# Optimization experiments

Hardware: AMD Instinct MI355X
Metric: run time of the kernel (lower is better)

Reference implementation:

```python
import jax, jax.numpy as jnp
import numpy as np

# pywt db4 decomposition filters
DEC_LO = jnp.array([-0.010597401784997278, 0.032883011666982945, 0.030841381835986965, -0.18703481171888114, -0.02798376941698385, 0.6308807679295904, 0.7148465705525415, 0.23037781330885523], dtype=jnp.float32)
DEC_HI = jnp.array([-0.23037781330885523, 0.7148465705525415, -0.6308807679295904, -0.02798376941698385, 0.18703481171888114, 0.030841381835986965, -0.032883011666982945, -0.010597401784997278], dtype=jnp.float32)

def _dwt_step(x):
    # single-level DWT along last axis, pywt 'symmetric' mode; x: [N, n]
    L = DEC_LO.shape[0]
    xe = jnp.pad(x, ((0, 0), (L - 1, L - 1)), mode='symmetric')[:, 1:]
    k = jnp.stack([DEC_LO[::-1], DEC_HI[::-1]])[:, None, :]  # [2,1,L]
    y = jax.lax.conv_general_dilated(xe[:, None, :], k, window_strides=(2,), padding='VALID')
    return y[:, 0, :], y[:, 1, :]  # cA, cD, each [N, (n+L-1)//2]

def _wavedec(x, level):
    a, dets = x, []
    for _ in range(level):
        a, d = _dwt_step(a)
        dets.append(d)
    return [a] + dets[::-1]  # [cA_L, cD_L, ..., cD_1]

def _wavelet_kan(x, basis, scales=5):
    # torch code detaches x before pywt.wavedec -> stop_gradient for faithful bwd
    coeffs = _wavedec(jax.lax.stop_gradient(x), scales - 1)
    out = 0.0
    for s in range(scales):
        c = coeffs[s]
        out = out + c @ basis[s][:c.shape[1], :]
    return out

def _dendritic(x, W, b):
    # W: [branches, in, out]; max over branches of GELU(Linear)
    h = jnp.einsum('ni,kio->kno', x, W) + b[:, None, :]
    return jnp.max(jax.nn.gelu(h, approximate=False), axis=0)

def _layernorm(x, g, b, eps=1e-5):
    m = jnp.mean(x, -1, keepdims=True)
    v = jnp.var(x, -1, keepdims=True)
    return (x - m) * jax.lax.rsqrt(v + eps) * g + b

def setup_inputs():
    key = jax.random.key(0)
    ks = jax.random.split(key, 12)
    N, D, H, M, Z, K, E = 16384, 768, 512, 256, 256, 20, 262144
    inp = {}
    inp['x'] = jax.random.normal(ks[0], (N, D), jnp.float32)
    inp['adj_rows'] = jax.random.randint(ks[1], (E,), 0, N, jnp.int32)
    inp['adj_cols'] = jax.random.randint(ks[2], (E,), 0, N, jnp.int32)
    inp['adj_vals'] = jax.random.uniform(ks[3], (E,), jnp.float32)
    inp['basis_enc'] = jax.random.normal(ks[4], (5, D, H), jnp.float32)
    inp['ln_g'] = jnp.ones((H,), jnp.float32)
    inp['ln_b'] = jnp.zeros((H,), jnp.float32)
    inp['Wd_enc'] = jax.random.normal(ks[5], (K, H, M), jnp.float32) * 0.04
    inp['bd_enc'] = jnp.zeros((K, M), jnp.float32)
    inp['W_mu'] = jax.random.normal(ks[6], (M, Z), jnp.float32) * 0.06
    inp['b_mu'] = jnp.zeros((Z,), jnp.float32)
    inp['W_lv'] = jax.random.normal(ks[7], (M, Z), jnp.float32) * 0.06
    inp['b_lv'] = jnp.zeros((Z,), jnp.float32)
    inp['Wd_dec'] = jax.random.normal(ks[8], (K, Z, H), jnp.float32) * 0.06
    inp['bd_dec'] = jnp.zeros((K, H), jnp.float32)
    inp['basis_dec'] = jax.random.normal(ks[9], (5, H, D), jnp.float32)
    inp['eps'] = jax.random.normal(ks[10], (N, Z), jnp.float32)
    return inp

def reference(x, adj_rows, adj_cols, adj_vals, basis_enc, ln_g, ln_b, Wd_enc, bd_enc, W_mu, b_mu, W_lv, b_lv, Wd_dec, bd_dec, basis_dec, eps):
    N = x.shape[0]
    # torch.sparse.mm(adj, x) with COO adj
    xa = jax.ops.segment_sum(adj_vals[:, None] * x[adj_cols], adj_rows, num_segments=N)
    h = _wavelet_kan(xa, basis_enc)
    h = _layernorm(h, ln_g, ln_b)
    enc = _dendritic(h, Wd_enc, bd_enc)
    mu = enc @ W_mu + b_mu
    logvar = enc @ W_lv + b_lv
    z = mu + eps * jnp.exp(0.5 * logvar)
    dec = _dendritic(z, Wd_dec, bd_dec)
    recon = _wavelet_kan(dec, basis_dec)
    return recon, mu, logvar
```

## Files before the change

### kernel.cpp

```cpp
#include <hip/hip_runtime.h>

typedef __attribute__((ext_vector_type(8))) short short8v;
typedef __attribute__((ext_vector_type(8))) unsigned short ushort8v;
typedef __attribute__((ext_vector_type(4))) float float4v;

__device__ __constant__ float c_LO[8] = {
    -0.010597401784997278f, 0.032883011666982945f, 0.030841381835986965f,
    -0.18703481171888114f, -0.02798376941698385f, 0.6308807679295904f,
    0.7148465705525415f, 0.23037781330885523f};
__device__ __constant__ float c_HI[8] = {
    -0.23037781330885523f, 0.7148465705525415f, -0.6308807679295904f,
    -0.02798376941698385f, 0.18703481171888114f, 0.030841381835986965f,
    -0.032883011666982945f, -0.010597401784997278f};

__device__ __forceinline__ unsigned short f2bf(float f) {
    unsigned u = __builtin_bit_cast(unsigned, f);
    unsigned r = u + 0x7fffu + ((u >> 16) & 1u);
    return (unsigned short)(r >> 16);
}
__device__ __forceinline__ float bf2f(unsigned short u) {
    return __builtin_bit_cast(float, (unsigned)u << 16);
}

__device__ __forceinline__ float gelu_fast(float x) {
    float x3 = x * x * x;
    float y = fmaf(0.044715f, x3, x) * 0.7978845608028654f;
    float t = fminf(fmaxf(y * 2.8853900817779268f, -30.f), 30.f);
    float e = exp2f(t);
    return x * e * __builtin_amdgcn_rcpf(e + 1.0f);
}

__device__ __forceinline__ void gload_lds16(const void* g, void* l) {
    __builtin_amdgcn_global_load_lds(g, l, 16, 0, 0);
}

__device__ __forceinline__ void dwt_lvl(const float* __restrict__ in, int n, float* __restrict__ outA,
                                        unsigned short* __restrict__ outD, int m, int lane) {
    for (int j = lane; j < m; j += 64) {
        float a = 0.f, d = 0.f;
#pragma unroll
        for (int i = 0; i < 8; ++i) {
            int p = 2 * j + 7 - i;
            int q = (p < 6) ? (5 - p) : ((p < n + 6) ? (p - 6) : (2 * n + 5 - p));
            float xv = in[q];
            a = fmaf(c_LO[i], xv, a);
            d = fmaf(c_HI[i], xv, d);
        }
        outA[j] = a;
        outD[j] = f2bf(d);
    }
}
__device__ __forceinline__ void dwt_lvl_final(const float* __restrict__ in, int n, unsigned short* __restrict__ outA,
                                              unsigned short* __restrict__ outD, int m, int lane) {
    for (int j = lane; j < m; j += 64) {
        float a = 0.f, d = 0.f;
#pragma unroll
        for (int i = 0; i < 8; ++i) {
            int p = 2 * j + 7 - i;
            int q = (p < 6) ? (5 - p) : ((p < n + 6) ? (p - 6) : (2 * n + 5 - p));
            float xv = in[q];
            a = fmaf(c_LO[i], xv, a);
            d = fmaf(c_HI[i], xv, d);
        }
        outA[j] = f2bf(a);
        outD[j] = f2bf(d);
    }
}

struct Bounds { int b[6]; };

__device__ __forceinline__ void job_pack_w(const float* __restrict__ W, unsigned short* __restrict__ WT,
                                           int br, int k0, int n0, int K, int N, int Kpad,
                                           float (*t)[65], int tid) {
#pragma unroll
    for (int i = 0; i < 16; ++i) {
        int idx = tid + i * 256;
        int kk = idx >> 6, nn = idx & 63;
        int k = k0 + kk;
        t[kk][nn] = (k < K) ? W[((size_t)br * K + k) * N + n0 + nn] : 0.f;
    }
    __syncthreads();
#pragma unroll
    for (int i = 0; i < 16; ++i) {
        int idx = tid + i * 256;
        int nn = idx >> 6, kk = idx & 63;
        int k = k0 + kk;
        if (k < Kpad)
            WT[((size_t)br * N + n0 + nn) * Kpad + k] = f2bf(t[kk][nn]);
    }
}

__device__ __forceinline__ void job_pack_basis(const float* __restrict__ basis, unsigned short* __restrict__ BT,
                                               Bounds bd, int brows, int N, int K, int Kpad,
                                               int k0, int n0, float (*t)[65], int tid) {
#pragma unroll
    for (int i = 0; i < 16; ++i) {
        int idx = tid + i * 256;
        int kk = idx >> 6, nn = idx & 63;
        int k = k0 + kk;
        float v = 0.f;
        if (k < K) {
            int s = 0;
#pragma unroll
            for (int u = 1; u < 5; ++u)
                if (k >= bd.b[u]) s = u;
            int lr = k - bd.b[s];
            v = basis[((size_t)s * brows + lr) * N + n0 + nn];
        }
        t[kk][nn] = v;
    }
    __syncthreads();
#pragma unroll
    for (int i = 0; i < 16; ++i) {
        int idx = tid + i * 256;
        int nn = idx >> 6, kk = idx & 63;
        int k = k0 + kk;
        if (k < Kpad)
            BT[(size_t)(n0 + nn) * Kpad + k] = f2bf(t[kk][nn]);
    }
}

__global__ __launch_bounds__(256) void prep_kernel(const float* __restrict__ x,
                                                   const float* __restrict__ basisenc,
                                                   const float* __restrict__ basisdec,
                                                   const float* __restrict__ Wd_enc,
                                                   const float* __restrict__ Wd_dec,
                                                   const float* __restrict__ W_mu,
                                                   const float* __restrict__ W_lv,
                                                   const int* __restrict__ arows, int E,
                                                   unsigned short* __restrict__ cenc,
                                                   unsigned short* __restrict__ BceT,
                                                   unsigned short* __restrict__ BcdT,
                                                   unsigned short* __restrict__ WdencT,
                                                   unsigned short* __restrict__ WddecT,
                                                   unsigned short* __restrict__ WmuT,
                                                   unsigned short* __restrict__ WlvT,
                                                   int* __restrict__ csr_cnt) {
    __shared__ __align__(16) char smem[18688];
    const int bid = blockIdx.x;
    const int tid = threadIdx.x;
    float (*t)[65] = (float(*)[65])smem;

    if (bid < 104) {
        Bounds be = {{0, 54, 108, 210, 407, 794}};
        int b = bid;
        job_pack_basis(basisenc, BceT, be, 768, 512, 794, 800, (b % 13) * 64, (b / 13) * 64, t, tid);
    } else if (bid < 212) {
        Bounds bdd = {{0, 38, 76, 146, 279, 538}};
        int b = bid - 104;
        job_pack_basis(basisdec, BcdT, bdd, 512, 768, 538, 544, (b % 9) * 64, (b / 9) * 64, t, tid);
    } else if (bid < 852) {
        int b = bid - 212;
        int br = b / 32, rem = b % 32;
        job_pack_w(Wd_enc, WdencT, br, (rem % 8) * 64, (rem / 8) * 64, 512, 256, 512, t, tid);
    } else if (bid < 1492) {
        int b = bid - 852;
        int br = b / 32, rem = b % 32;
        job_pack_w(Wd_dec, WddecT, br, (rem % 4) * 64, (rem / 4) * 64, 256, 512, 256, t, tid);
    } else if (bid < 1508) {
        int b = bid - 1492;
        job_pack_w(W_mu, WmuT, 0, (b % 4) * 64, (b / 4) * 64, 256, 256, 256, t, tid);
    } else if (bid < 1524) {
        int b = bid - 1508;
        job_pack_w(W_lv, WlvT, 0, (b % 4) * 64, (b / 4) * 64, 256, 256, 256, t, tid);
    } else if (bid < 5620) {
        const int widx = tid >> 6, lane = tid & 63;
        const int r = (bid - 1524) * 4 + widx;
        float* b0 = (float*)smem + widx * 1168;
        float* b1 = b0 + 768;
        const float* ip = x + (size_t)r * 768;
        for (int i = lane; i < 768; i += 64) b0[i] = ip[i];
        __syncthreads();
        unsigned short* cr = cenc + (size_t)r * 800;
        dwt_lvl(b0, 768, b1, cr + 407, 387, lane);
        __syncthreads();
        dwt_lvl(b1, 387, b0, cr + 210, 197, lane);
        __syncthreads();
        dwt_lvl(b0, 197, b1, cr + 108, 102, lane);
        __syncthreads();
        dwt_lvl_final(b1, 102, cr + 0, cr + 54, 54, lane);
        if (lane < 6) cr[794 + lane] = 0;
    } else {
        int i = (bid - 5620) * 256 + tid;
        if (i < E) atomicAdd(&csr_cnt[arows[i]], 1);
    }
}

__global__ __launch_bounds__(1024) void scan_kernel(const int* __restrict__ cnt, int* __restrict__ offs,
                                                    int* __restrict__ cursor, int Nrows, int E) {
    __shared__ int part[1024];
    int tid = threadIdx.x;
    const int per = Nrows / 1024;
    int base = tid * per;
    int local[16];
    int s = 0;
    for (int i = 0; i < per; ++i) { local[i] = s; s += cnt[base + i]; }
    part[tid] = s;
    __syncthreads();
    for (int off = 1; off < 1024; off <<= 1) {
        int v = part[tid];
        int w = (tid >= off) ? part[tid - off] : 0;
        __syncthreads();
        part[tid] = v + w;
        __syncthreads();
    }
    int pre = (tid == 0) ? 0 : part[tid - 1];
    for (int i = 0; i < per; ++i) {
        int o = pre + local[i];
        offs[base + i] = o;
        cursor[base + i] = o;
    }
    if (tid == 0) offs[Nrows] = E;
}

__global__ void scatter_kernel(const int* __restrict__ rows, const int* __restrict__ cols,
                               const float* __restrict__ vals, int* __restrict__ cursor,
                               int* __restrict__ ccol, float* __restrict__ cval, int E) {
    int i = blockIdx.x * blockDim.x + threadIdx.x;
    if (i >= E) return;
    int r = rows[i];
    int p = atomicAdd(&cursor[r], 1);
    ccol[p] = cols[i];
    cval[p] = vals[i];
}

__global__ __launch_bounds__(256) void spmm_ln(const unsigned short* __restrict__ hx,
                                               const int* __restrict__ offs,
                                               const int* __restrict__ ccol,
                                               const float* __restrict__ cval,
                                               const float* __restrict__ g,
                                               const float* __restrict__ b,
                                               unsigned short* __restrict__ hbf) {
    const int widx = threadIdx.x >> 6, lane = threadIdx.x & 63;
    const int r = blockIdx.x * 4 + widx;
    int s = offs[r], e = offs[r + 1];
    float acc[8] = {}, acc2[8] = {};
    int j = s;
    for (; j + 1 < e; j += 2) {
        int c0 = ccol[j], c1 = ccol[j + 1];
        float v0 = cval[j], v1 = cval[j + 1];
        ushort8v u0 = *(const ushort8v*)(hx + (size_t)c0 * 512 + lane * 8);
        ushort8v u1 = *(const ushort8v*)(hx + (size_t)c1 * 512 + lane * 8);
#pragma unroll
        for (int t = 0; t < 8; ++t) {
            acc[t] = fmaf(v0, bf2f(u0[t]), acc[t]);
            acc2[t] = fmaf(v1, bf2f(u1[t]), acc2[t]);
        }
    }
    if (j < e) {
        int c0 = ccol[j];
        float v0 = cval[j];
        ushort8v u0 = *(const ushort8v*)(hx + (size_t)c0 * 512 + lane * 8);
#pragma unroll
        for (int t = 0; t < 8; ++t) acc[t] = fmaf(v0, bf2f(u0[t]), acc[t]);
    }
#pragma unroll
    for (int t = 0; t < 8; ++t) acc[t] += acc2[t];

    float s1 = 0.f, s2 = 0.f;
#pragma unroll
    for (int t = 0; t < 8; ++t) { s1 += acc[t]; s2 = fmaf(acc[t], acc[t], s2); }
#pragma unroll
    for (int off = 32; off >= 1; off >>= 1) {
        s1 += __shfl_xor(s1, off);
        s2 += __shfl_xor(s2, off);
    }
    float mean = s1 * (1.f / 512.f);
    float var = s2 * (1.f / 512.f) - mean * mean;
    float inv = rsqrtf(var + 1e-5f);
    ushort8v o;
#pragma unroll
    for (int t = 0; t < 8; ++t) {
        int col = lane * 8 + t;
        o[t] = f2bf((acc[t] - mean) * inv * g[col] + b[col]);
    }
    *(ushort8v*)(hbf + (size_t)r * 512 + lane * 8) = o;
}

__global__ __launch_bounds__(256) void wavedec_dec(const unsigned short* __restrict__ decb,
                                                   unsigned short* __restrict__ cdec) {
    __shared__ float buf0[4][512];
    __shared__ float buf1[4][272];
    const int widx = threadIdx.x >> 6, lane = threadIdx.x & 63;
    const int r = blockIdx.x * 4 + widx;
    float* b0 = buf0[widx];
    float* b1 = buf1[widx];
    const unsigned short* ip = decb + (size_t)r * 512;
    for (int i = lane; i < 512; i += 64) b0[i] = bf2f(ip[i]);
    __syncthreads();
    unsigned short* cr = cdec + (size_t)r * 544;
    dwt_lvl(b0, 512, b1, cr + 279, 259, lane);
    __syncthreads();
    dwt_lvl(b1, 259, b0, cr + 146, 133, lane);
    __syncthreads();
    dwt_lvl(b0, 133, b1, cr + 76, 70, lane);
    __syncthreads();
    dwt_lvl_final(b1, 70, cr + 0, cr + 38, 38, lane);
    if (lane < 6) cr[538 + lane] = 0;
}

template <int MODE>
__global__ __launch_bounds__(256) void gemm_mfma(const unsigned short* __restrict__ A,
                                                 const unsigned short* __restrict__ BT,
                                                 const float* __restrict__ bias,
                                                 const float* __restrict__ bias2,
                                                 void* __restrict__ Cv, void* __restrict__ Cv2,
                                                 int M, int N, int K, int lda, int ldb, int ldc, int nx) {
    __shared__ __align__(16) unsigned short As[128 * 32];
    __shared__ __align__(16) unsigned short Bs[128 * 32];
    const int tid = threadIdx.x;
    const int wave = tid >> 6, lane = tid & 63;
    const int nwg = gridDim.x;
    const int logical = (blockIdx.x & 7) * (nwg >> 3) + (blockIdx.x >> 3);
    const int mblk = logical / nx, nblk = logical - mblk * nx;
    const int m0 = mblk * 128, n0 = nblk * 128;
    const int wr = wave >> 1, wc = wave & 1;
    const int frow = lane & 15, fq = lane >> 4;

    const int off0 = tid * 16;
    const int r0 = off0 >> 6, c0 = off0 & 63;
    const int r1 = (off0 + 4096) >> 6, c1 = (off0 + 4096) & 63;
    const char* Ab = (const char*)A;
    const char* Bb = (const char*)BT;
    size_t gA0 = (size_t)(m0 + r0) * lda * 2 + c0;
    size_t gA1 = (size_t)(m0 + r1) * lda * 2 + c1;
    size_t gB0 = (size_t)(n0 + r0) * ldb * 2 + c0;
    size_t gB1 = (size_t)(n0 + r1) * ldb * 2 + c1;
    char* lA0 = (char*)As + wave * 1024;
    char* lB0 = (char*)Bs + wave * 1024;

    const int aoff = (wr * 64 + frow) * 32 + fq * 8;
    const int boff = (wc * 64 + frow) * 32 + fq * 8;

    float4v acc[4][4] = {};
    for (int k0 = 0; k0 < K; k0 += 32) {
        size_t kb2 = (size_t)k0 * 2;
        gload_lds16(Ab + gA0 + kb2, lA0);
        gload_lds16(Ab + gA1 + kb2, lA0 + 4096);
        gload_lds16(Bb + gB0 + kb2, lB0);
        gload_lds16(Bb + gB1 + kb2, lB0 + 4096);
        __syncthreads();
        short8v av[4], bv[4];
#pragma unroll
        for (int i = 0; i < 4; ++i) av[i] = *(const short8v*)(As + aoff + i * 512);
#pragma unroll
        for (int i = 0; i < 4; ++i) bv[i] = *(const short8v*)(Bs + boff + i * 512);
#pragma unroll
        for (int mi = 0; mi < 4; ++mi)
#pragma unroll
            for (int ni = 0; ni < 4; ++ni)
                acc[mi][ni] = __builtin_amdgcn_mfma_f32_16x16x32_bf16(av[mi], bv[ni], acc[mi][ni], 0, 0, 0);
        __syncthreads();
    }
#pragma unroll
    for (int ni = 0; ni < 4; ++ni) {
        int col = n0 + wc * 64 + ni * 16 + frow;
#pragma unroll
        for (int mi = 0; mi < 4; ++mi) {
#pragma unroll
            for (int i = 0; i < 4; ++i) {
                int row = m0 + wr * 64 + mi * 16 + fq * 4 + i;
                if (MODE == 0) {
                    ((float*)Cv)[(size_t)row * ldc + col] = acc[mi][ni][i];
                } else if (MODE == 1) {
                    ((unsigned short*)Cv)[(size_t)row * ldc + col] = f2bf(acc[mi][ni][i]);
                } else {
                    bool isMu = col < 256;
                    int coll = col & 255;
                    float bval = isMu ? bias[coll] : bias2[coll];
                    float* dst = (float*)(isMu ? Cv : Cv2);
                    dst[(size_t)row * 256 + coll] = acc[mi][ni][i] + bval;
                }
            }
        }
    }
}

__global__ void z_kernel(const float* __restrict__ mu, const float* __restrict__ lv,
                         const float* __restrict__ eps, unsigned short* __restrict__ z, int n4) {
    int i = blockIdx.x * blockDim.x + threadIdx.x;
    if (i >= n4) return;
    float4 m = ((const float4*)mu)[i];
    float4 l = ((const float4*)lv)[i];
    float4 e = ((const float4*)eps)[i];
    ushort4 o;
    o.x = f2bf(m.x + e.x * expf(0.5f * l.x));
    o.y = f2bf(m.y + e.y * expf(0.5f * l.y));
    o.z = f2bf(m.z + e.z * expf(0.5f * l.z));
    o.w = f2bf(m.w + e.w * expf(0.5f * l.w));
    ((ushort4*)z)[i] = o;
}

__global__ __launch_bounds__(256, 2) void dendritic_full(const unsigned short* __restrict__ A,
                                                         const unsigned short* __restrict__ WT,
                                                         const float* __restrict__ bias,
                                                         unsigned short* __restrict__ out,
                                                         int M, int Nc, int K, int nb, int nx) {
    __shared__ __align__(16) unsigned short As[128 * 64];
    __shared__ __align__(16) unsigned short Bs[2][64 * 64];
    const int tid = threadIdx.x;
    const int wave = tid >> 6;
    const int lane = tid & 63;

    const int nwg = gridDim.x;
    const int logical = (blockIdx.x & 7) * (nwg >> 3) + (blockIdx.x >> 3);
    const int mblk = logical / nx;
    const int nblk = logical - mblk * nx;
    const int n0 = nblk * 64, m0 = mblk * 128;

    const int wr = wave >> 1, wc = wave & 1;
    const int frow = lane & 15, fq = lane >> 4;

    int srA[4], scA[4];
#pragma unroll
    for (int i = 0; i < 4; ++i) {
        int ch = i * 256 + tid;
        srA[i] = ch >> 3;
        scA[i] = ((ch & 7) ^ (srA[i] & 7)) * 16;
    }
    int srB[2], scB[2];
#pragma unroll
    for (int i = 0; i < 2; ++i) {
        int ch = i * 256 + tid;
        srB[i] = ch >> 3;
        scB[i] = ((ch & 7) ^ (srB[i] & 7)) * 16;
    }
    const char* Ab = (const char*)A;
    const size_t K2 = (size_t)K * 2;
    const size_t branchBytes = (size_t)Nc * K2;
    char* lA  = (char*)As + wave * 1024;
    char* lB0 = (char*)&Bs[0][0] + wave * 1024;
    char* lB1 = (char*)&Bs[1][0] + wave * 1024;

    float4v hmn[4][2], hmx[4][2];
#pragma unroll
    for (int mi = 0; mi < 4; ++mi)
#pragma unroll
        for (int ni = 0; ni < 2; ++ni) { hmn[mi][ni] = (float4v)(1e30f); hmx[mi][ni] = (float4v)(-1e30f); }

    const int npair = nb >> 1;
    for (int p = 0; p < npair; ++p) {
        const int b0 = 2 * p, b1 = 2 * p + 1;
        const char* Bb0 = (const char*)WT + (size_t)b0 * branchBytes;
        const char* Bb1 = (const char*)WT + (size_t)b1 * branchBytes;
        float4v ac0[4][2], ac1[4][2];
#pragma unroll
        for (int ni = 0; ni < 2; ++ni) {
            int col = n0 + wc * 32 + ni * 16 + frow;
            float bv0 = bias[(size_t)b0 * Nc + col];
            float bv1 = bias[(size_t)b1 * Nc + col];
#pragma unroll
            for (int mi = 0; mi < 4; ++mi) { ac0[mi][ni] = (float4v)(bv0); ac1[mi][ni] = (float4v)(bv1); }
        }
        for (int k0 = 0; k0 < K; k0 += 64) {
            const size_t kby = (size_t)k0 * 2;
#pragma unroll
            for (int i = 0; i < 4; ++i)
                gload_lds16(Ab + (size_t)(m0 + srA[i]) * K2 + kby + scA[i], lA + i * 4096);
#pragma unroll
            for (int i = 0; i < 2; ++i)
                gload_lds16(Bb0 + (size_t)(n0 + srB[i]) * K2 + kby + scB[i], lB0 + i * 4096);
#pragma unroll
            for (int i = 0; i < 2; ++i)
                gload_lds16(Bb1 + (size_t)(n0 + srB[i]) * K2 + kby + scB[i], lB1 + i * 4096);
            __syncthreads();
#pragma unroll
            for (int kk = 0; kk < 2; ++kk) {
                short8v av[4], bv0[2], bv1[2];
                const int slot = kk * 4 + fq;
#pragma unroll
                for (int mi = 0; mi < 4; ++mi) {
                    int ra = wr * 64 + mi * 16 + frow;
                    av[mi] = *(const short8v*)((const char*)As + ra * 128 + ((slot ^ (ra & 7)) * 16));
                }
#pragma unroll
                for (int ni = 0; ni < 2; ++ni) {
                    int rb = wc * 32 + ni * 16 + frow;
                    int rboff = rb * 128 + ((slot ^ (rb & 7)) * 16);
                    bv0[ni] = *(const short8v*)((const char*)&Bs[0][0] + rboff);
                    bv1[ni] = *(const short8v*)((const char*)&Bs[1][0] + rboff);
                }
#pragma unroll
                for (int mi = 0; mi < 4; ++mi)
#pragma unroll
                    for (int ni = 0; ni < 2; ++ni) {
                        ac0[mi][ni] = __builtin_amdgcn_mfma_f32_16x16x32_bf16(av[mi], bv0[ni], ac0[mi][ni], 0, 0, 0);
                        ac1[mi][ni] = __builtin_amdgcn_mfma_f32_16x16x32_bf16(av[mi], bv1[ni], ac1[mi][ni], 0, 0, 0);
                    }
            }
            __syncthreads();
        }
#pragma unroll
        for (int ni = 0; ni < 2; ++ni)
#pragma unroll
            for (int mi = 0; mi < 4; ++mi)
#pragma unroll
                for (int i = 0; i < 4; ++i) {
                    float mn = fminf(ac0[mi][ni][i], ac1[mi][ni][i]);
                    float mx = fmaxf(ac0[mi][ni][i], ac1[mi][ni][i]);
                    hmn[mi][ni][i] = fminf(hmn[mi][ni][i], mn);
                    hmx[mi][ni][i] = fmaxf(hmx[mi][ni][i], mx);
                }
    }

#pragma unroll
    for (int ni = 0; ni < 2; ++ni) {
        int col = n0 + wc * 32 + ni * 16 + frow;
#pragma unroll
        for (int mi = 0; mi < 4; ++mi) {
#pragma unroll
            for (int i = 0; i < 4; ++i) {
                int row = m0 + wr * 64 + mi * 16 + fq * 4 + i;
                float g = fmaxf(gelu_fast(hmn[mi][ni][i]), gelu_fast(hmx[mi][ni][i]));
                out[(size_t)row * Nc + col] = f2bf(g);
            }
        }
    }
}

__global__ __launch_bounds__(256, 2) void dendritic_dec_res(const unsigned short* __restrict__ A,
                                                            const unsigned short* __restrict__ WT,
                                                            const float* __restrict__ bias,
                                                            unsigned short* __restrict__ out,
                                                            int M, int Nc, int nb, int nx) {
    constexpr int K = 256;
    __shared__ __align__(16) unsigned short As[128 * 256];
    __shared__ __align__(16) unsigned short Bs[2][64 * 64];
    const int tid = threadIdx.x;
    const int wave = tid >> 6;
    const int lane = tid & 63;

    const int nwg = gridDim.x;
    const int logical = (blockIdx.x & 7) * (nwg >> 3) + (blockIdx.x >> 3);
    const int mblk = logical / nx;
    const int nblk = logical - mblk * nx;
    const int n0 = nblk * 64, m0 = mblk * 128;

    const int wr = wave >> 1, wc = wave & 1;
    const int frow = lane & 15, fq = lane >> 4;

    const char* Ab = (const char*)A;
    const size_t K2 = (size_t)K * 2;
    for (int i = 0; i < 16; ++i) {
        int ch = i * 256 + tid;
        int row = ch >> 5, slot = ch & 31;
        int sslot = (slot & ~7) | ((slot & 7) ^ (row & 7));
        gload_lds16(Ab + (size_t)(m0 + row) * K2 + sslot * 16, (char*)As + i * 4096 + wave * 1024);
    }

    int srB[2], scB[2];
#pragma unroll
    for (int i = 0; i < 2; ++i) {
        int ch = i * 256 + tid;
        srB[i] = ch >> 3;
        scB[i] = ((ch & 7) ^ (srB[i] & 7)) * 16;
    }
    const size_t branchBytes = (size_t)Nc * K2;
    char* lB0 = (char*)&Bs[0][0] + wave * 1024;
    char* lB1 = (char*)&Bs[1][0] + wave * 1024;

    float4v hmn[4][2], hmx[4][2];
#pragma unroll
    for (int mi = 0; mi < 4; ++mi)
#pragma unroll
        for (int ni = 0; ni < 2; ++ni) { hmn[mi][ni] = (float4v)(1e30f); hmx[mi][ni] = (float4v)(-1e30f); }

    const int npair = nb >> 1;
    for (int p = 0; p < npair; ++p) {
        const int b0 = 2 * p, b1 = 2 * p + 1;
        const char* Bb0 = (const char*)WT + (size_t)b0 * branchBytes;
        const char* Bb1 = (const char*)WT + (size_t)b1 * branchBytes;
        float4v ac0[4][2], ac1[4][2];
#pragma unroll
        for (int ni = 0; ni < 2; ++ni) {
            int col = n0 + wc * 32 + ni * 16 + frow;
            float bv0 = bias[(size_t)b0 * Nc + col];
            float bv1 = bias[(size_t)b1 * Nc + col];
#pragma unroll
            for (int mi = 0; mi < 4; ++mi) { ac0[mi][ni] = (float4v)(bv0); ac1[mi][ni] = (float4v)(bv1); }
        }
        for (int k0 = 0; k0 < K; k0 += 64) {
            const size_t kby = (size_t)k0 * 2;
#pragma unroll
            for (int i = 0; i < 2; ++i)
                gload_lds16(Bb0 + (size_t)(n0 + srB[i]) * K2 + kby + scB[i], lB0 + i * 4096);
#pragma unroll
            for (int i = 0; i < 2; ++i)
                gload_lds16(Bb1 + (size_t)(n0 + srB[i]) * K2 + kby + scB[i], lB1 + i * 4096);
            __syncthreads();
#pragma unroll
            for (int kk = 0; kk < 2; ++kk) {
                short8v av[4], bv0[2], bv1[2];
                const int slot = kk * 4 + fq;
#pragma unroll
                for (int mi = 0; mi < 4; ++mi) {
                    int ra = wr * 64 + mi * 16 + frow;
                    int g = (k0 >> 3) + slot;
                    int sl = (g & ~7) | ((g & 7) ^ (ra & 7));
                    av[mi] = *(const short8v*)((const char*)As + ra * 512 + sl * 16);
                }
#pragma unroll
                for (int ni = 0; ni < 2; ++ni) {
                    int rb = wc * 32 + ni * 16 + frow;
                    int rboff = rb * 128 + ((slot ^ (rb & 7)) * 16);
                    bv0[ni] = *(const short8v*)((const char*)&Bs[0][0] + rboff);
                    bv1[ni] = *(const short8v*)((const char*)&Bs[1][0] + rboff);
                }
#pragma unroll
                for (int mi = 0; mi < 4; ++mi)
#pragma unroll
                    for (int ni = 0; ni < 2; ++ni) {
                        ac0[mi][ni] = __builtin_amdgcn_mfma_f32_16x16x32_bf16(av[mi], bv0[ni], ac0[mi][ni], 0, 0, 0);
                        ac1[mi][ni] = __builtin_amdgcn_mfma_f32_16x16x32_bf16(av[mi], bv1[ni], ac1[mi][ni], 0, 0, 0);
                    }
            }
            __syncthreads();
        }
#pragma unroll
        for (int ni = 0; ni < 2; ++ni)
#pragma unroll
            for (int mi = 0; mi < 4; ++mi)
#pragma unroll
                for (int i = 0; i < 4; ++i) {
                    float mn = fminf(ac0[mi][ni][i], ac1[mi][ni][i]);
                    float mx = fmaxf(ac0[mi][ni][i], ac1[mi][ni][i]);
                    hmn[mi][ni][i] = fminf(hmn[mi][ni][i], mn);
                    hmx[mi][ni][i] = fmaxf(hmx[mi][ni][i], mx);
                }
    }

#pragma unroll
    for (int ni = 0; ni < 2; ++ni) {
        int col = n0 + wc * 32 + ni * 16 + frow;
#pragma unroll
        for (int mi = 0; mi < 4; ++mi) {
#pragma unroll
            for (int i = 0; i < 4; ++i) {
                int row = m0 + wr * 64 + mi * 16 + fq * 4 + i;
                float g = fmaxf(gelu_fast(hmn[mi][ni][i]), gelu_fast(hmx[mi][ni][i]));
                out[(size_t)row * Nc + col] = f2bf(g);
            }
        }
    }
}

extern "C" void kernel_launch(void* const* d_in, const int* in_sizes, int n_in,
                              void* d_out, int out_size, void* d_ws, size_t ws_size,
                              hipStream_t stream) {
    const float* x        = (const float*)d_in[0];
    const int*   arows    = (const int*)d_in[1];
    const int*   acols    = (const int*)d_in[2];
    const float* avals    = (const float*)d_in[3];
    const float* basisenc = (const float*)d_in[4];
    const float* ln_g     = (const float*)d_in[5];
    const float* ln_b     = (const float*)d_in[6];
    const float* Wd_enc   = (const float*)d_in[7];
    const float* bd_enc   = (const float*)d_in[8];
    const float* W_mu     = (const float*)d_in[9];
    const float* b_mu     = (const float*)d_in[10];
    const float* W_lv     = (const float*)d_in[11];
    const float* b_lv     = (const float*)d_in[12];
    const float* Wd_dec   = (const float*)d_in[13];
    const float* bd_dec   = (const float*)d_in[14];
    const float* basisdec = (const float*)d_in[15];
    const float* epsin    = (const float*)d_in[16];

    const int N = 16384;
    const int E = in_sizes[1];

    float* ws = (float*)d_ws;
    const size_t A0 = 0;
    const size_t B0 = A0 + (size_t)N * 768;
    const size_t C0 = B0 + (size_t)N * 400;
    const size_t F0 = C0 + (size_t)N * 387;
    const size_t G0 = F0 + 3100672;

    unsigned short* hx   = (unsigned short*)(ws + A0);
    unsigned short* cenc = (unsigned short*)(ws + B0);
    unsigned short* cdec = (unsigned short*)(ws + B0);
    unsigned short* zb   = cdec + (size_t)N * 544;
    unsigned short* hbf  = (unsigned short*)(ws + C0);
    unsigned short* encb = hbf + (size_t)N * 512;
    unsigned short* decb = (unsigned short*)(ws + C0);
    unsigned short* wF = (unsigned short*)(ws + F0);
    unsigned short* BceT   = wF;
    unsigned short* BcdT   = BceT + 512 * 800;
    unsigned short* WdencT = BcdT + 768 * 544;
    unsigned short* WddecT = WdencT + 20 * 256 * 512;
    unsigned short* WmuT   = WddecT + 20 * 512 * 256;
    unsigned short* WlvT   = WmuT + 256 * 256;
    int*   csr_cnt  = (int*)(ws + G0);
    int*   csr_offs = csr_cnt + N;
    int*   csr_cur  = csr_offs + N + 1;
    int*   csr_col  = csr_cur + N;
    float* csr_val  = (float*)(csr_col + E);

    float* out_recon = (float*)d_out;
    float* out_mu    = out_recon + (size_t)N * 768;
    float* out_lv    = out_mu + (size_t)N * 256;

    hipMemsetAsync(csr_cnt, 0, N * sizeof(int), stream);
    {
        const int nwgPrep = 104 + 108 + 640 + 640 + 16 + 16 + (N / 4) + (E + 255) / 256;
        prep_kernel<<<nwgPrep, 256, 0, stream>>>(x, basisenc, basisdec, Wd_enc, Wd_dec, W_mu, W_lv,
                                                 arows, E, cenc, BceT, BcdT, WdencT, WddecT, WmuT, WlvT,
                                                 csr_cnt);
    }
    scan_kernel<<<1, 1024, 0, stream>>>(csr_cnt, csr_offs, csr_cur, N, E);
    scatter_kernel<<<(E + 255) / 256, 256, 0, stream>>>(arows, acols, avals, csr_cur, csr_col, csr_val, E);

    gemm_mfma<1><<<(512 / 128) * (N / 128), 256, 0, stream>>>(cenc, BceT, nullptr, nullptr, hx, nullptr,
                                                              N, 512, 800, 800, 800, 512, 512 / 128);

    spmm_ln<<<N / 4, 256, 0, stream>>>(hx, csr_offs, csr_col, csr_val, ln_g, ln_b, hbf);

    dendritic_full<<<4 * (N / 128), 256, 0, stream>>>(hbf, WdencT, bd_enc, encb, N, 256, 512, 20, 4);

    gemm_mfma<2><<<(512 / 128) * (N / 128), 256, 0, stream>>>(encb, WmuT, b_mu, b_lv, out_mu, out_lv,
                                                              N, 512, 256, 256, 256, 256, 512 / 128);

    z_kernel<<<(N * 256 / 4 + 255) / 256, 256, 0, stream>>>(out_mu, out_lv, epsin, zb, N * 256 / 4);

    dendritic_dec_res<<<8 * (N / 128), 256, 0, stream>>>(zb, WddecT, bd_dec, decb, N, 512, 20, 8);

    wavedec_dec<<<N / 4, 256, 0, stream>>>(decb, cdec);

    gemm_mfma<0><<<(768 / 128) * (N / 128), 256, 0, stream>>>(cdec, BcdT, nullptr, nullptr, out_recon, nullptr,
                                                              N, 768, 544, 544, 544, 768, 768 / 128);

    (void)ws_size; (void)out_size; (void)n_in;
}
```

Before: 392.5 us.

## Double-buffer LDS tiles in GEMM and dendritic kernels; unroll SpMM gather by four

The generic MFMA GEMM and the dendritic encoder kernel now double-buffer their LDS tiles. The next K-slice is issued into the alternate buffer before the MFMAs on the current one, so global-to-LDS loads overlap with compute and one barrier per step is dropped. The dendritic kernel flattens its branch-pair and K loops into one pipelined loop, so prefetch also crosses branch boundaries. The SpMM+LayerNorm gather keeps four independent rows in flight instead of two. Costs are doubled LDS use, which may reduce occupancy, and more registers in the gather.

```diff
diff --git a/kernel.cpp b/kernel.cpp
--- a/kernel.cpp
+++ b/kernel.cpp
@@ -234,28 +234,33 @@
     const int widx = threadIdx.x >> 6, lane = threadIdx.x & 63;
     const int r = blockIdx.x * 4 + widx;
     int s = offs[r], e = offs[r + 1];
-    float acc[8] = {}, acc2[8] = {};
+    float a0[8] = {}, a1[8] = {}, a2[8] = {}, a3[8] = {};
     int j = s;
-    for (; j + 1 < e; j += 2) {
-        int c0 = ccol[j], c1 = ccol[j + 1];
-        float v0 = cval[j], v1 = cval[j + 1];
+    for (; j + 3 < e; j += 4) {
+        int c0 = ccol[j], c1 = ccol[j + 1], c2 = ccol[j + 2], c3 = ccol[j + 3];
+        float v0 = cval[j], v1 = cval[j + 1], v2 = cval[j + 2], v3 = cval[j + 3];
         ushort8v u0 = *(const ushort8v*)(hx + (size_t)c0 * 512 + lane * 8);
         ushort8v u1 = *(const ushort8v*)(hx + (size_t)c1 * 512 + lane * 8);
+        ushort8v u2 = *(const ushort8v*)(hx + (size_t)c2 * 512 + lane * 8);
+        ushort8v u3 = *(const ushort8v*)(hx + (size_t)c3 * 512 + lane * 8);
 #pragma unroll
         for (int t = 0; t < 8; ++t) {
-            acc[t] = fmaf(v0, bf2f(u0[t]), acc[t]);
-            acc2[t] = fmaf(v1, bf2f(u1[t]), acc2[t]);
-        }
-    }
-    if (j < e) {
+            a0[t] = fmaf(v0, bf2f(u0[t]), a0[t]);
+            a1[t] = fmaf(v1, bf2f(u1[t]), a1[t]);
+            a2[t] = fmaf(v2, bf2f(u2[t]), a2[t]);
+            a3[t] = fmaf(v3, bf2f(u3[t]), a3[t]);
+        }
+    }
+    for (; j < e; ++j) {
         int c0 = ccol[j];
         float v0 = cval[j];
         ushort8v u0 = *(const ushort8v*)(hx + (size_t)c0 * 512 + lane * 8);
 #pragma unroll
-        for (int t = 0; t < 8; ++t) acc[t] = fmaf(v0, bf2f(u0[t]), acc[t]);
-    }
-#pragma unroll
-    for (int t = 0; t < 8; ++t) acc[t] += acc2[t];
+        for (int t = 0; t < 8; ++t) a0[t] = fmaf(v0, bf2f(u0[t]), a0[t]);
+    }
+    float acc[8];
+#pragma unroll
+    for (int t = 0; t < 8; ++t) acc[t] = (a0[t] + a1[t]) + (a2[t] + a3[t]);
 
     float s1 = 0.f, s2 = 0.f;
 #pragma unroll
@@ -306,8 +311,8 @@
                                                  const float* __restrict__ bias2,
                                                  void* __restrict__ Cv, void* __restrict__ Cv2,
                                                  int M, int N, int K, int lda, int ldb, int ldc, int nx) {
-    __shared__ __align__(16) unsigned short As[128 * 32];
-    __shared__ __align__(16) unsigned short Bs[128 * 32];
+    __shared__ __align__(16) unsigned short As[2 * 128 * 32];
+    __shared__ __align__(16) unsigned short Bs[2 * 128 * 32];
     const int tid = threadIdx.x;
     const int wave = tid >> 6, lane = tid & 63;
     const int nwg = gridDim.x;
@@ -326,31 +331,41 @@
     size_t gA1 = (size_t)(m0 + r1) * lda * 2 + c1;
     size_t gB0 = (size_t)(n0 + r0) * ldb * 2 + c0;
     size_t gB1 = (size_t)(n0 + r1) * ldb * 2 + c1;
-    char* lA0 = (char*)As + wave * 1024;
-    char* lB0 = (char*)Bs + wave * 1024;
 
     const int aoff = (wr * 64 + frow) * 32 + fq * 8;
     const int boff = (wc * 64 + frow) * 32 + fq * 8;
-
+    const int KS = K >> 5;
+
+    auto stage = [&](int ks, int buf) {
+        size_t kb2 = (size_t)ks * 64;
+        char* lA = (char*)As + buf * 8192 + wave * 1024;
+        char* lB = (char*)Bs + buf * 8192 + wave * 1024;
+        gload_lds16(Ab + gA0 + kb2, lA);
+        gload_lds16(Ab + gA1 + kb2, lA + 4096);
+        gload_lds16(Bb + gB0 + kb2, lB);
+        gload_lds16(Bb + gB1 + kb2, lB + 4096);
+    };
+
+    stage(0, 0);
+    __syncthreads();
     float4v acc[4][4] = {};
-    for (int k0 = 0; k0 < K; k0 += 32) {
-        size_t kb2 = (size_t)k0 * 2;
-        gload_lds16(Ab + gA0 + kb2, lA0);
-        gload_lds16(Ab + gA1 + kb2, lA0 + 4096);
-        gload_lds16(Bb + gB0 + kb2, lB0);
-        gload_lds16(Bb + gB1 + kb2, lB0 + 4096);
-        __syncthreads();
+    int buf = 0;
+    for (int ks = 0; ks < KS; ++ks) {
+        if (ks + 1 < KS) stage(ks + 1, buf ^ 1);
+        const unsigned short* Ap = As + buf * 4096;
+        const unsigned short* Bp = Bs + buf * 4096;
         short8v av[4], bv[4];
 #pragma unroll
-        for (int i = 0; i < 4; ++i) av[i] = *(const short8v*)(As + aoff + i * 512);
-#pragma unroll
-        for (int i = 0; i < 4; ++i) bv[i] = *(const short8v*)(Bs + boff + i * 512);
+        for (int i = 0; i < 4; ++i) av[i] = *(const short8v*)(Ap + aoff + i * 512);
+#pragma unroll
+        for (int i = 0; i < 4; ++i) bv[i] = *(const short8v*)(Bp + boff + i * 512);
 #pragma unroll
         for (int mi = 0; mi < 4; ++mi)
 #pragma unroll
             for (int ni = 0; ni < 4; ++ni)
                 acc[mi][ni] = __builtin_amdgcn_mfma_f32_16x16x32_bf16(av[mi], bv[ni], acc[mi][ni], 0, 0, 0);
         __syncthreads();
+        buf ^= 1;
     }
 #pragma unroll
     for (int ni = 0; ni < 4; ++ni) {
@@ -396,8 +411,8 @@
                                                          const float* __restrict__ bias,
                                                          unsigned short* __restrict__ out,
                                                          int M, int Nc, int K, int nb, int nx) {
-    __shared__ __align__(16) unsigned short As[128 * 64];
-    __shared__ __align__(16) unsigned short Bs[2][64 * 64];
+    __shared__ __align__(16) unsigned short As[2 * 128 * 64];
+    __shared__ __align__(16) unsigned short Bs[2][2][64 * 64];
     const int tid = threadIdx.x;
     const int wave = tid >> 6;
     const int lane = tid & 63;
@@ -428,9 +443,27 @@
     const char* Ab = (const char*)A;
     const size_t K2 = (size_t)K * 2;
     const size_t branchBytes = (size_t)Nc * K2;
-    char* lA  = (char*)As + wave * 1024;
-    char* lB0 = (char*)&Bs[0][0] + wave * 1024;
-    char* lB1 = (char*)&Bs[1][0] + wave * 1024;
+    const int KS = K >> 6;
+    const int T = (nb >> 1) * KS;
+
+    auto stage = [&](int t, int buf) {
+        int pr = t / KS, ks = t - pr * KS;
+        size_t kby = (size_t)ks * 128;
+        const char* Bb0 = (const char*)WT + (size_t)(2 * pr) * branchBytes;
+        const char* Bb1 = (const char*)WT + (size_t)(2 * pr + 1) * branchBytes;
+        char* lA  = (char*)As + buf * 16384 + wave * 1024;
+        char* lB0 = (char*)&Bs[buf][0][0] + wave * 1024;
+        char* lB1 = (char*)&Bs[buf][1][0] + wave * 1024;
+#pragma unroll
+        for (int i = 0; i < 4; ++i)
+            gload_lds16(Ab + (size_t)(m0 + srA[i]) * K2 + kby + scA[i], lA + i * 4096);
+#pragma unroll
+        for (int i = 0; i < 2; ++i)
+            gload_lds16(Bb0 + (size_t)(n0 + srB[i]) * K2 + kby + scB[i], lB0 + i * 4096);
+#pragma unroll
+        for (int i = 0; i < 2; ++i)
+            gload_lds16(Bb1 + (size_t)(n0 + srB[i]) * K2 + kby + scB[i], lB1 + i * 4096);
+    };
 
     float4v hmn[4][2], hmx[4][2];
 #pragma unroll
@@ -438,69 +471,63 @@
 #pragma unroll
         for (int ni = 0; ni < 2; ++ni) { hmn[mi][ni] = (float4v)(1e30f); hmx[mi][ni] = (float4v)(-1e30f); }
 
-    const int npair = nb >> 1;
-    for (int p = 0; p < npair; ++p) {
-        const int b0 = 2 * p, b1 = 2 * p + 1;
-        const char* Bb0 = (const char*)WT + (size_t)b0 * branchBytes;
-        const char* Bb1 = (const char*)WT + (size_t)b1 * branchBytes;
-        float4v ac0[4][2], ac1[4][2];
-#pragma unroll
-        for (int ni = 0; ni < 2; ++ni) {
-            int col = n0 + wc * 32 + ni * 16 + frow;
-            float bv0 = bias[(size_t)b0 * Nc + col];
-            float bv1 = bias[(size_t)b1 * Nc + col];
-#pragma unroll
-            for (int mi = 0; mi < 4; ++mi) { ac0[mi][ni] = (float4v)(bv0); ac1[mi][ni] = (float4v)(bv1); }
-        }
-        for (int k0 = 0; k0 < K; k0 += 64) {
-            const size_t kby = (size_t)k0 * 2;
-#pragma unroll
-            for (int i = 0; i < 4; ++i)
-                gload_lds16(Ab + (size_t)(m0 + srA[i]) * K2 + kby + scA[i], lA + i * 4096);
-#pragma unroll
-            for (int i = 0; i < 2; ++i)
-                gload_lds16(Bb0 + (size_t)(n0 + srB[i]) * K2 + kby + scB[i], lB0 + i * 4096);
-#pragma unroll
-            for (int i = 0; i < 2; ++i)
-                gload_lds16(Bb1 + (size_t)(n0 + srB[i]) * K2 + kby + scB[i], lB1 + i * 4096);
-            __syncthreads();
-#pragma unroll
-            for (int kk = 0; kk < 2; ++kk) {
-                short8v av[4], bv0[2], bv1[2];
-                const int slot = kk * 4 + fq;
-#pragma unroll
-                for (int mi = 0; mi < 4; ++mi) {
-                    int ra = wr * 64 + mi * 16 + frow;
-                    av[mi] = *(const short8v*)((const char*)As + ra * 128 + ((slot ^ (ra & 7)) * 16));
+    float4v ac0[4][2], ac1[4][2];
+    stage(0, 0);
+    __syncthreads();
+    int buf = 0;
+    for (int t = 0; t < T; ++t) {
+        const int pr = t / KS, ks = t - pr * KS;
+        if (ks == 0) {
+#pragma unroll
+            for (int ni = 0; ni < 2; ++ni) {
+                int col = n0 + wc * 32 + ni * 16 + frow;
+                float bv0 = bias[(size_t)(2 * pr) * Nc + col];
+                float bv1 = bias[(size_t)(2 * pr + 1) * Nc + col];
+#pragma unroll
+                for (int mi = 0; mi < 4; ++mi) { ac0[mi][ni] = (float4v)(bv0); ac1[mi][ni] = (float4v)(bv1); }
+            }
+        }
+        if (t + 1 < T) stage(t + 1, buf ^ 1);
+        const char* Ap = (const char*)As + buf * 16384;
+#pragma unroll
+        for (int kk = 0; kk < 2; ++kk) {
+            short8v av[4], bv0[2], bv1[2];
+            const int slot = kk * 4 + fq;
+#pragma unroll
+            for (int mi = 0; mi < 4; ++mi) {
+                int ra = wr * 64 + mi * 16 + frow;
+                av[mi] = *(const short8v*)(Ap + ra * 128 + ((slot ^ (ra & 7)) * 16));
+            }
+#pragma unroll
+            for (int ni = 0; ni < 2; ++ni) {
+                int rb = wc * 32 + ni * 16 + frow;
+                int rboff = rb * 128 + ((slot ^ (rb & 7)) * 16);
+                bv0[ni] = *(const short8v*)((const char*)&Bs[buf][0][0] + rboff);
+                bv1[ni] = *(const short8v*)((const char*)&Bs[buf][1][0] + rboff);
+            }
+#pragma unroll
+            for (int mi = 0; mi < 4; ++mi)
+#pragma unroll
+                for (int ni = 0; ni < 2; ++ni) {
+                    ac0[mi][ni] = __builtin_amdgcn_mfma_f32_16x16x32_bf16(av[mi], bv0[ni], ac0[mi][ni], 0, 0, 0);
+                    ac1[mi][ni] = __builtin_amdgcn_mfma_f32_16x16x32_bf16(av[mi], bv1[ni], ac1[mi][ni], 0, 0, 0);
                 }
-#pragma unroll
-                for (int ni = 0; ni < 2; ++ni) {
-                    int rb = wc * 32 + ni * 16 + frow;
-                    int rboff = rb * 128 + ((slot ^ (rb & 7)) * 16);
-                    bv0[ni] = *(const short8v*)((const char*)&Bs[0][0] + rboff);
-                    bv1[ni] = *(const short8v*)((const char*)&Bs[1][0] + rboff);
-                }
+        }
+        if (ks == KS - 1) {
+#pragma unroll
+            for (int ni = 0; ni < 2; ++ni)
 #pragma unroll
                 for (int mi = 0; mi < 4; ++mi)
 #pragma unroll
-                    for (int ni = 0; ni < 2; ++ni) {
-                        ac0[mi][ni] = __builtin_amdgcn_mfma_f32_16x16x32_bf16(av[mi], bv0[ni], ac0[mi][ni], 0, 0, 0);
-                        ac1[mi][ni] = __builtin_amdgcn_mfma_f32_16x16x32_bf16(av[mi], bv1[ni], ac1[mi][ni], 0, 0, 0);
+                    for (int i = 0; i < 4; ++i) {
+                        float mn = fminf(ac0[mi][ni][i], ac1[mi][ni][i]);
+                        float mx = fmaxf(ac0[mi][ni][i], ac1[mi][ni][i]);
+                        hmn[mi][ni][i] = fminf(hmn[mi][ni][i], mn);
+                        hmx[mi][ni][i] = fmaxf(hmx[mi][ni][i], mx);
                     }
-            }
-            __syncthreads();
-        }
-#pragma unroll
-        for (int ni = 0; ni < 2; ++ni)
-#pragma unroll
-            for (int mi = 0; mi < 4; ++mi)
-#pragma unroll
-                for (int i = 0; i < 4; ++i) {
-                    float mn = fminf(ac0[mi][ni][i], ac1[mi][ni][i]);
-                    float mx = fmaxf(ac0[mi][ni][i], ac1[mi][ni][i]);
-                    hmn[mi][ni][i] = fminf(hmn[mi][ni][i], mn);
-                    hmx[mi][ni][i] = fmaxf(hmx[mi][ni][i], mx);
-                }
+        }
+        __syncthreads();
+        buf ^= 1;
     }
 
 #pragma unroll
```

Measured after the change: 394.2 us. Within noise of the previous version (+0.4%).
